# Optimization experiments

Hardware: AMD Instinct MI355X
Metric: run time of the kernel (lower is better)

The kernel has to match this reference:

```python
import jax, jax.numpy as jnp
import numpy as np

B, N, D = 2, 1024, 512
H, DH = 8, 64
HD = H * DH
FF = 2048
DEPTH = 4
SCALE = DH ** -0.5


def layer_norm(x, g, b, eps=1e-5):
    m = jnp.mean(x, axis=-1, keepdims=True)
    v = jnp.mean((x - m) ** 2, axis=-1, keepdims=True)
    return (x - m) / jnp.sqrt(v + eps) * g + b


def rel_shift(x):
    # x: (i, j, b, h) -> Transformer-XL relative shift via pad/reshape/slice
    i, j = x.shape[0], x.shape[1]
    zp = jnp.zeros((i, 1) + x.shape[2:], x.dtype)
    xp = jnp.concatenate([zp, x], axis=1).reshape((j + 1, i) + x.shape[2:])
    return xp[1:].reshape(x.shape)


def setup_inputs() -> dict:
    key = jax.random.key(0)
    ks = jax.random.split(key, 20)
    s = 0.02
    inp = {
        'x':   jax.random.normal(ks[0], (B, N, D), jnp.float32),
        'r_t': jax.random.normal(ks[1], (B, N, D), jnp.float32),
        'r_c': jax.random.normal(ks[2], (B, N, D), jnp.float32),
        'r_p': jax.random.normal(ks[3], (B, N, D), jnp.float32),
        'bias_pf': jax.random.normal(ks[4], (H, DH), jnp.float32) * s,
        'ln1_g': jnp.ones((DEPTH, D), jnp.float32),
        'ln1_b': jnp.zeros((DEPTH, D), jnp.float32),
        'w_qkv': jax.random.normal(ks[5], (DEPTH, D, 3 * HD), jnp.float32) * s,
        'w_out': jax.random.normal(ks[6], (DEPTH, HD, D), jnp.float32) * s,
        'b_out': jnp.zeros((DEPTH, D), jnp.float32),
        'w_kt': jax.random.normal(ks[7], (DEPTH, D, HD), jnp.float32) * s,
        'w_kc': jax.random.normal(ks[8], (DEPTH, D, HD), jnp.float32) * s,
        'w_kp': jax.random.normal(ks[9], (DEPTH, D, HD), jnp.float32) * s,
        'ln2_g': jnp.ones((DEPTH, D), jnp.float32),
        'ln2_b': jnp.zeros((DEPTH, D), jnp.float32),
        'w_ff1': jax.random.normal(ks[10], (DEPTH, D, FF), jnp.float32) * s,
        'b_ff1': jnp.zeros((DEPTH, FF), jnp.float32),
        'w_ff2': jax.random.normal(ks[11], (DEPTH, FF, D), jnp.float32) * s,
        'b_ff2': jnp.zeros((DEPTH, D), jnp.float32),
    }
    return inp


def _to_nbhd(t, b, n):
    # (b, n, h*d) -> (n, b, h, d)
    return t.reshape(b, n, H, DH).transpose(1, 0, 2, 3)


def reference(x, r_t, r_c, r_p, bias_pf, ln1_g, ln1_b, w_qkv, w_out, b_out,
              w_kt, w_kc, w_kp, ln2_g, ln2_b, w_ff1, b_ff1, w_ff2, b_ff2):
    b, n, _ = x.shape
    attn_last = None
    for l in range(DEPTH):
        xn = layer_norm(x, ln1_g[l], ln1_b[l])
        qkv = xn @ w_qkv[l]  # (b, n, 3*HD)
        q, k, v = jnp.split(qkv, 3, axis=-1)
        q = _to_nbhd(q, b, n) + bias_pf  # Ex_Wq + bias_pf, (n,b,h,d)
        k = _to_nbhd(k, b, n)
        v = _to_nbhd(v, b, n)
        wt = _to_nbhd(r_t @ w_kt[l], b, n)
        wc = _to_nbhd(r_c @ w_kc[l], b, n)
        wp = _to_nbhd(r_p @ w_kp[l], b, n)
        AC = jnp.einsum('ibhd,jbhd->ijbh', q, k)
        BD = (rel_shift(jnp.einsum('ibhd,jbhd->ijbh', q, wt))
              + rel_shift(jnp.einsum('ibhd,jbhd->ijbh', q, wc))
              + rel_shift(jnp.einsum('ibhd,jbhd->ijbh', q, wp))) * (1.0 / 3.0)
        dots = (AC + BD) * SCALE
        # NOTE: source uses nn.Softmax(dim=-1) on (i,j,b,h), i.e. over heads.
        attn = jax.nn.softmax(dots, axis=-1)
        out = jnp.einsum('ijbh,jbhd->ibhd', attn, v)
        out = out.transpose(1, 0, 2, 3).reshape(b, n, HD)
        x = out @ w_out[l] + b_out[l] + x
        xn2 = layer_norm(x, ln2_g[l], ln2_b[l])
        h1 = jax.nn.gelu(xn2 @ w_ff1[l] + b_ff1[l], approximate=False)
        x = h1 @ w_ff2[l] + b_ff2[l] + x
        attn_last = attn
    # attention rearranged 'q k b h -> b h q k'
    return x, attn_last.transpose(2, 3, 0, 1)
```

## Files before the change

### kernel.cpp

```cpp
#include <hip/hip_runtime.h>
#include <hip/hip_bf16.h>


using bf16 = __hip_bfloat16;
typedef __attribute__((ext_vector_type(8))) short short8;
typedef __attribute__((ext_vector_type(4))) float float4v;
typedef __attribute__((ext_vector_type(2))) unsigned int uint2v;

__device__ __forceinline__ float ldsel(const void* p, long long i, bool isbf) {
    return isbf ? __bfloat162float(((const bf16*)p)[i]) : ((const float*)p)[i];
}
__device__ __forceinline__ void stsel(void* p, long long i, bool isbf, float v) {
    if (isbf) ((bf16*)p)[i] = __float2bfloat16(v);
    else      ((float*)p)[i] = v;
}
__device__ __forceinline__ float bf2f(short u) {
    return __uint_as_float(((unsigned)(unsigned short)u) << 16);
}
__device__ __forceinline__ short f2bf(float f) {
    bf16 h = __float2bfloat16(f);
    return *reinterpret_cast<short*>(&h);
}

__global__ void detect_kernel(const unsigned int* __restrict__ g, int* __restrict__ flag) {
    if (threadIdx.x == 0) flag[0] = ((g[0] & 0xFFFFu) != 0u) ? 1 : 0;
}

__global__ __launch_bounds__(256) void cast_in(const void* __restrict__ in, float* __restrict__ out,
                                               int n8, const int* __restrict__ flagp) {
    bool bf = flagp[0] != 0;
    int i = blockIdx.x * 256 + threadIdx.x;
    if (i >= n8) return;
    long long b = (long long)i * 8;
    if (bf) {
        short8 v = *(const short8*)((const bf16*)in + b);
        float4v o0, o1;
        #pragma unroll
        for (int j = 0; j < 4; ++j) { o0[j] = bf2f(v[j]); o1[j] = bf2f(v[4 + j]); }
        *(float4v*)(out + b) = o0;
        *(float4v*)(out + b + 4) = o1;
    } else {
        float4v a0 = *(const float4v*)((const float*)in + b);
        float4v a1 = *(const float4v*)((const float*)in + b + 4);
        *(float4v*)(out + b) = a0;
        *(float4v*)(out + b + 4) = a1;
    }
}
__global__ __launch_bounds__(256) void cast_out(const float* __restrict__ in, void* __restrict__ out,
                                                int n8, const int* __restrict__ flagp) {
    bool bf = flagp[0] != 0;
    int i = blockIdx.x * 256 + threadIdx.x;
    if (i >= n8) return;
    long long b = (long long)i * 8;
    float4v a0 = *(const float4v*)(in + b);
    float4v a1 = *(const float4v*)(in + b + 4);
    if (bf) {
        short8 v;
        #pragma unroll
        for (int j = 0; j < 4; ++j) { v[j] = f2bf(a0[j]); v[4 + j] = f2bf(a1[j]); }
        *(short8*)((bf16*)out + b) = v;
    } else {
        *(float4v*)((float*)out + b) = a0;
        *(float4v*)((float*)out + b + 4) = a1;
    }
}

__global__ __launch_bounds__(256) void attn_out(const bf16* __restrict__ attn,
                                                void* __restrict__ out,
                                                const int* __restrict__ flagp) {
    bool bf = flagp[0] != 0;
    long long e = ((long long)blockIdx.x * 256 + threadIdx.x) * 8;
    short8 v = *(const short8*)(attn + e);
    if (bf) {
        *(short8*)((bf16*)out + 1048576 + e) = v;
    } else {
        float4v o0, o1;
        #pragma unroll
        for (int j = 0; j < 4; ++j) { o0[j] = bf2f(v[j]); o1[j] = bf2f(v[4 + j]); }
        float* op = (float*)out + 1048576 + e;
        *(float4v*)op = o0;
        *(float4v*)(op + 4) = o1;
    }
}

__global__ __launch_bounds__(256) void rcat_all(const void* __restrict__ r0, const void* __restrict__ r1,
                                                const void* __restrict__ r2, bf16* __restrict__ dst,
                                                const int* __restrict__ flagp) {
    bool bf = flagp[0] != 0;
    int s = blockIdx.y;
    const void* src = (s == 0) ? r0 : ((s == 1) ? r1 : r2);
    int i = blockIdx.x * 256 + threadIdx.x;
    int m = i >> 6, k8 = (i & 63) * 8;
    long long b = (long long)m * 512 + k8;
    short8 v;
    if (bf) {
        v = *(const short8*)((const bf16*)src + b);
    } else {
        float4v a0 = *(const float4v*)((const float*)src + b);
        float4v a1 = *(const float4v*)((const float*)src + b + 4);
        #pragma unroll
        for (int j = 0; j < 4; ++j) { v[j] = f2bf(a0[j]); v[4 + j] = f2bf(a1[j]); }
    }
    *(short8*)(dst + (size_t)m * 1536 + s * 512 + k8) = v;
}

__global__ __launch_bounds__(256) void prep_weights(
    const void* __restrict__ s0, const void* __restrict__ s1, const void* __restrict__ s2,
    const void* __restrict__ s3, const void* __restrict__ s4, const void* __restrict__ s5,
    const void* __restrict__ s6, bf16* __restrict__ arena,
    const int* __restrict__ flagp) {
    const bool bf = flagp[0] != 0;
    const int bid = blockIdx.x;
    const int l = bid / 960;
    const int rem = bid - l * 960;
    const int LW = 3932160;
    const int L = l * LW;

    int j, tile, tx, ldi, ldo;
    long long ioff;
    int dstoff;
    if (rem < 192)      { j = 0; tile = rem;                tx = 24; ldi = 1536; ldo = 512;
                          ioff = (long long)l * 786432;  dstoff = L; }
    else if (rem < 448) { j = 1 + ((rem - 192) >> 6); tile = (rem - 192) & 63; tx = 8; ldi = 512;
                          ioff = (long long)l * 262144;
                          if (j <= 3) { ldo = 1536; dstoff = L + 786432 + (j - 1) * 512; }
                          else        { ldo = 512;  dstoff = L + 1572864; } }
    else if (rem < 704) { j = 5; tile = rem - 448;          tx = 32; ldi = 2048; ldo = 512;
                          ioff = (long long)l * 1048576; dstoff = L + 1835008; }
    else                { j = 6; tile = rem - 704;          tx = 8;  ldi = 512;  ldo = 2048;
                          ioff = (long long)l * 1048576; dstoff = L + 2883584; }
    const void* in = (j == 0) ? s0 : (j == 1) ? s1 : (j == 2) ? s2 :
                     (j == 3) ? s3 : (j == 4) ? s4 : (j == 5) ? s5 : s6;
    bf16* out = arena + dstoff;
    const int bx = tile % tx, by = tile / tx;
    const int n0 = bx * 64, k0 = by * 64;
    const int tid = threadIdx.x;

    __shared__ bf16 t[64][72];

    if (bf) {
        const bf16* inb = (const bf16*)in + ioff;
        #pragma unroll
        for (int p = 0; p < 2; ++p) {
            int e = tid + p * 256;
            int r = e >> 3, c = (e & 7) * 8;
            *(uint4*)&t[r][c] = *(const uint4*)(inb + (size_t)(k0 + r) * ldi + n0 + c);
        }
    } else {
        const float* inf = (const float*)in + ioff;
        #pragma unroll
        for (int p = 0; p < 4; ++p) {
            int e = tid + p * 256;
            int r = e >> 4, c = (e & 15) * 4;
            float4v v = *(const float4v*)(inf + (size_t)(k0 + r) * ldi + n0 + c);
            union { bf16 h[4]; uint2v u; } w;
            #pragma unroll
            for (int q = 0; q < 4; ++q) w.h[q] = __float2bfloat16(v[q]);
            *reinterpret_cast<uint2v*>(&t[r][c]) = w.u;
        }
    }
    __syncthreads();
    #pragma unroll
    for (int p = 0; p < 2; ++p) {
        int e = tid + p * 256;
        int r = e >> 3, c = (e & 7) * 8;
        union { short8 s; uint4 u; } o;
        #pragma unroll
        for (int q = 0; q < 8; ++q)
            o.s[q] = *reinterpret_cast<const short*>(&t[c + q][r]);
        *(uint4*)(out + (size_t)(n0 + r) * ldo + k0 + c) = o.u;
    }
}

__global__ __launch_bounds__(256) void ln_kernel(const float* __restrict__ x,
                                                 const void* __restrict__ g, long long goff,
                                                 const void* __restrict__ bta, long long boff,
                                                 bf16* __restrict__ out,
                                                 const int* __restrict__ flagp) {
    bool bf = flagp[0] != 0;
    int row = blockIdx.x;
    const float* xr = x + (size_t)row * 512;
    int tid = threadIdx.x;
    float v0 = xr[tid], v1 = xr[tid + 256];
    float s = v0 + v1, q = v0 * v0 + v1 * v1;
    #pragma unroll
    for (int off = 32; off; off >>= 1) {
        s += __shfl_down(s, off);
        q += __shfl_down(q, off);
    }
    __shared__ float ls[4], lq[4];
    int wid = tid >> 6, lane = tid & 63;
    if (lane == 0) { ls[wid] = s; lq[wid] = q; }
    __syncthreads();
    if (tid == 0) {
        float ts = ls[0] + ls[1] + ls[2] + ls[3];
        float tq = lq[0] + lq[1] + lq[2] + lq[3];
        float m = ts * (1.f / 512.f);
        float var = tq * (1.f / 512.f) - m * m;
        ls[0] = m; lq[0] = rsqrtf(var + 1e-5f);
    }
    __syncthreads();
    float m = ls[0], r = lq[0];
    out[(size_t)row * 512 + tid] =
        __float2bfloat16((v0 - m) * r * ldsel(g, goff + tid, bf) + ldsel(bta, boff + tid, bf));
    out[(size_t)row * 512 + tid + 256] =
        __float2bfloat16((v1 - m) * r * ldsel(g, goff + tid + 256, bf) + ldsel(bta, boff + tid + 256, bf));
}

template<int EPI>
__global__ __launch_bounds__(256) void mgemm(
    const bf16* __restrict__ A, int lda, long long sAb, long long sAh,
    const bf16* __restrict__ B, int ldb, long long sBb, long long sBh,
    void* __restrict__ Cv, int ldc, long long sCb, long long sCh,
    int K,
    const void* __restrict__ bias, long long biasoff,
    float* __restrict__ resid,
    bf16* __restrict__ aux,
    const int* __restrict__ flagp) {
    const bool flg = flagp[0] != 0;
    const int tid = threadIdx.x;
    const int lane = tid & 63, wave = tid >> 6;
    const int m0 = blockIdx.y * 128, n0 = blockIdx.x * 64;
    const int zb = (int)(blockIdx.z >> 3), zh = (int)(blockIdx.z & 7);
    A += (size_t)zb * sAb + (size_t)zh * sAh;
    B += (size_t)zb * sBb + (size_t)zh * sBh;

    __shared__ bf16 As[128][40];
    __shared__ bf16 Bs[64][40];

    const int ar = tid >> 2, ak = (tid & 3) * 8;
    const bf16* Ap0 = A + (size_t)(m0 + ar) * lda + ak;
    const bf16* Ap1 = Ap0 + (size_t)64 * lda;
    const bf16* Bp  = B + (size_t)(n0 + ar) * ldb + ak;

    const int wm = (wave >> 1) * 64, wn = (wave & 1) * 32;
    const int fr = lane & 15, fq = lane >> 4;

    float4v acc[4][2] = {};

    uint4 a0 = *(const uint4*)Ap0;
    uint4 a1 = *(const uint4*)Ap1;
    uint4 b0 = *(const uint4*)Bp;

    for (int k0 = 0; k0 < K; k0 += 32) {
        __syncthreads();
        *(uint4*)&As[ar][ak]      = a0;
        *(uint4*)&As[ar + 64][ak] = a1;
        *(uint4*)&Bs[ar][ak]      = b0;
        if (k0 + 32 < K) {
            a0 = *(const uint4*)(Ap0 + k0 + 32);
            a1 = *(const uint4*)(Ap1 + k0 + 32);
            b0 = *(const uint4*)(Bp + k0 + 32);
        }
        __syncthreads();
        union { uint4 u; short8 s; } ua[4], ub[2];
        #pragma unroll
        for (int i = 0; i < 4; ++i) ua[i].u = *(const uint4*)&As[wm + i * 16 + fr][fq * 8];
        #pragma unroll
        for (int j = 0; j < 2; ++j) ub[j].u = *(const uint4*)&Bs[wn + j * 16 + fr][fq * 8];
        #pragma unroll
        for (int i = 0; i < 4; ++i)
            #pragma unroll
            for (int j = 0; j < 2; ++j)
                acc[i][j] = __builtin_amdgcn_mfma_f32_16x16x32_bf16(ua[i].s, ub[j].s, acc[i][j], 0, 0, 0);
    }

    const long long coff = (long long)zb * sCb + (long long)zh * sCh;
    #pragma unroll
    for (int i = 0; i < 4; ++i) {
        #pragma unroll
        for (int j = 0; j < 2; ++j) {
            #pragma unroll
            for (int r = 0; r < 4; ++r) {
                int m = m0 + wm + i * 16 + fq * 4 + r;
                int n = n0 + wn + j * 16 + fr;
                float v = acc[i][j][r];
                if (EPI == 1) {
                    bf16* C = (bf16*)Cv;
                    if (n < 512) {
                        C[(size_t)m * ldc + n] = __float2bfloat16(v + ldsel(bias, biasoff + n, flg));
                    } else if (n < 1024) {
                        C[(size_t)m * ldc + n] = __float2bfloat16(v);
                    } else {
                        int h = (n >> 6) & 7, d = n & 63, ii = m & 1023, bb = m >> 10;
                        aux[(size_t)(bb * 8 + h) * 65536 + (size_t)d * 1024 + ii] = __float2bfloat16(v);
                    }
                } else if (EPI == 2) {
                    float* C = (float*)Cv;
                    C[(size_t)m * ldc + n] = v + ldsel(bias, biasoff + n, flg) + resid[(size_t)m * ldc + n];
                } else if (EPI == 3) {
                    bf16* C = (bf16*)Cv;
                    float t = v + ldsel(bias, biasoff + n, flg);
                    C[(size_t)m * ldc + n] = __float2bfloat16(0.5f * t * (1.f + erff(t * 0.70710678118f)));
                } else if (EPI == 5) {
                    bf16* C = (bf16*)Cv + coff;
                    C[(size_t)m * ldc + n] = __float2bfloat16(v);
                }
            }
        }
    }
}

template<int EPI>
__global__ __launch_bounds__(256) void mgemm64(
    const bf16* __restrict__ A, int lda, long long sAb, long long sAh,
    const bf16* __restrict__ B, int ldb, long long sBb, long long sBh,
    void* __restrict__ Cv, int ldc, long long sCb, long long sCh,
    int K,
    const void* __restrict__ bias, long long biasoff,
    float* __restrict__ resid,
    bf16* __restrict__ aux,
    const int* __restrict__ flagp) {
    const bool flg = flagp[0] != 0;
    const int tid = threadIdx.x;
    const int lane = tid & 63, wave = tid >> 6;
    const int m0 = blockIdx.y * 64, n0 = blockIdx.x * 64;
    const int zb = (int)(blockIdx.z >> 3), zh = (int)(blockIdx.z & 7);
    A += (size_t)zb * sAb + (size_t)zh * sAh;
    B += (size_t)zb * sBb + (size_t)zh * sBh;

    __shared__ bf16 As[64][40];
    __shared__ bf16 Bs[64][40];

    const int ar = tid >> 2, ak = (tid & 3) * 8;
    const bf16* Ap = A + (size_t)(m0 + ar) * lda + ak;
    const bf16* Bp = B + (size_t)(n0 + ar) * ldb + ak;

    const int wm = (wave >> 1) * 32, wn = (wave & 1) * 32;
    const int fr = lane & 15, fq = lane >> 4;

    float4v acc[2][2] = {};

    uint4 a0 = *(const uint4*)Ap;
    uint4 b0 = *(const uint4*)Bp;

    for (int k0 = 0; k0 < K; k0 += 32) {
        __syncthreads();
        *(uint4*)&As[ar][ak] = a0;
        *(uint4*)&Bs[ar][ak] = b0;
        if (k0 + 32 < K) {
            a0 = *(const uint4*)(Ap + k0 + 32);
            b0 = *(const uint4*)(Bp + k0 + 32);
        }
        __syncthreads();
        union { uint4 u; short8 s; } ua[2], ub[2];
        #pragma unroll
        for (int i = 0; i < 2; ++i) ua[i].u = *(const uint4*)&As[wm + i * 16 + fr][fq * 8];
        #pragma unroll
        for (int j = 0; j < 2; ++j) ub[j].u = *(const uint4*)&Bs[wn + j * 16 + fr][fq * 8];
        #pragma unroll
        for (int i = 0; i < 2; ++i)
            #pragma unroll
            for (int j = 0; j < 2; ++j)
                acc[i][j] = __builtin_amdgcn_mfma_f32_16x16x32_bf16(ua[i].s, ub[j].s, acc[i][j], 0, 0, 0);
    }

    const long long coff = (long long)zb * sCb + (long long)zh * sCh;
    #pragma unroll
    for (int i = 0; i < 2; ++i) {
        #pragma unroll
        for (int j = 0; j < 2; ++j) {
            #pragma unroll
            for (int r = 0; r < 4; ++r) {
                int m = m0 + wm + i * 16 + fq * 4 + r;
                int n = n0 + wn + j * 16 + fr;
                float v = acc[i][j][r];
                if (EPI == 1) {
                    bf16* C = (bf16*)Cv;
                    if (n < 512) {
                        C[(size_t)m * ldc + n] = __float2bfloat16(v + ldsel(bias, biasoff + n, flg));
                    } else if (n < 1024) {
                        C[(size_t)m * ldc + n] = __float2bfloat16(v);
                    } else {
                        int h = (n >> 6) & 7, d = n & 63, ii = m & 1023, bb = m >> 10;
                        aux[(size_t)(bb * 8 + h) * 65536 + (size_t)d * 1024 + ii] = __float2bfloat16(v);
                    }
                } else if (EPI == 2) {
                    float* C = (float*)Cv;
                    C[(size_t)m * ldc + n] = v + ldsel(bias, biasoff + n, flg) + resid[(size_t)m * ldc + n];
                } else if (EPI == 5) {
                    bf16* C = (bf16*)Cv + coff;
                    C[(size_t)m * ldc + n] = __float2bfloat16(v);
                }
            }
        }
    }
}

__global__ __launch_bounds__(512) void bd_kernel(
    const bf16* __restrict__ qkvb, const bf16* __restrict__ wsum,
    bf16* __restrict__ Scb) {
    const int tid = threadIdx.x;
    const int lane = tid & 63, wave = tid >> 6;
    const int n0 = blockIdx.x * 64, m0 = blockIdx.y * 64, b = blockIdx.z;

    __shared__ bf16 Qs[64][72];
    __shared__ bf16 Ws[64][72];

    const int r0 = tid >> 3, c0 = (tid & 7) * 8;
    const bf16* Qp = qkvb + (size_t)(b * 1024 + m0 + r0) * 1536 + c0;
    const bf16* Wp = wsum + (size_t)(b * 1024 + n0 + r0) * 512 + c0;

    const int wm = (wave >> 2) * 32, wn = (wave & 3) * 16;
    const int fr = lane & 15, fq = lane >> 4;

    float4v acc[8][2] = {};

    uint4 qreg = *(const uint4*)Qp;
    uint4 wreg = *(const uint4*)Wp;

    for (int h = 0; h < 8; ++h) {
        __syncthreads();
        *(uint4*)&Qs[r0][c0] = qreg;
        *(uint4*)&Ws[r0][c0] = wreg;
        if (h < 7) {
            qreg = *(const uint4*)(Qp + (h + 1) * 64);
            wreg = *(const uint4*)(Wp + (h + 1) * 64);
        }
        __syncthreads();
        #pragma unroll
        for (int ks = 0; ks < 2; ++ks) {
            union { uint4 u; short8 s; } ua[2], ub;
            #pragma unroll
            for (int i = 0; i < 2; ++i) ua[i].u = *(const uint4*)&Qs[wm + i * 16 + fr][fq * 8 + ks * 32];
            ub.u = *(const uint4*)&Ws[wn + fr][fq * 8 + ks * 32];
            #pragma unroll
            for (int i = 0; i < 2; ++i)
                acc[h][i] = __builtin_amdgcn_mfma_f32_16x16x32_bf16(ua[i].s, ub.s, acc[h][i], 0, 0, 0);
        }
    }

    const size_t pb = (size_t)b * 8388608;
    #pragma unroll
    for (int i = 0; i < 2; ++i) {
        #pragma unroll
        for (int r = 0; r < 4; ++r) {
            int m = m0 + wm + i * 16 + fq * 4 + r;
            int n = n0 + wn + fr;
            int t = m * 1025 + n + 1;
            if (t >= 1024) {
                short8 v;
                #pragma unroll
                for (int h = 0; h < 8; ++h) v[h] = f2bf(acc[h][i][r] * (1.f / 3.f));
                *(short8*)(Scb + pb + (size_t)(t - 1024) * 8) = v;
            }
        }
    }
}

__global__ __launch_bounds__(512) void scores_kernel(
    const bf16* __restrict__ qkvb, const bf16* __restrict__ Scb,
    bf16* __restrict__ attn) {
    const int tid = threadIdx.x;
    const int lane = tid & 63, wave = tid >> 6;
    const int j0 = blockIdx.x * 64, i0 = blockIdx.y * 64, b = blockIdx.z;

    __shared__ bf16 Qs[64][72];
    __shared__ bf16 Ks[64][72];

    const int r0 = tid >> 3, c0 = (tid & 7) * 8;
    const bf16* Qp = qkvb + (size_t)(b * 1024 + i0 + r0) * 1536 + c0;
    const bf16* Kp = qkvb + (size_t)(b * 1024 + j0 + r0) * 1536 + 512 + c0;

    const int wm = (wave >> 2) * 32, wn = (wave & 3) * 16;
    const int fr = lane & 15, fq = lane >> 4;

    float4v acc[8][2] = {};

    uint4 qreg = *(const uint4*)Qp;
    uint4 kreg = *(const uint4*)Kp;

    for (int h = 0; h < 8; ++h) {
        __syncthreads();
        *(uint4*)&Qs[r0][c0] = qreg;
        *(uint4*)&Ks[r0][c0] = kreg;
        if (h < 7) {
            qreg = *(const uint4*)(Qp + (h + 1) * 64);
            kreg = *(const uint4*)(Kp + (h + 1) * 64);
        }
        __syncthreads();
        #pragma unroll
        for (int ks = 0; ks < 2; ++ks) {
            union { uint4 u; short8 s; } ua[2], ub;
            #pragma unroll
            for (int i = 0; i < 2; ++i) ua[i].u = *(const uint4*)&Qs[wm + i * 16 + fr][fq * 8 + ks * 32];
            ub.u = *(const uint4*)&Ks[wn + fr][fq * 8 + ks * 32];
            #pragma unroll
            for (int i = 0; i < 2; ++i)
                acc[h][i] = __builtin_amdgcn_mfma_f32_16x16x32_bf16(ua[i].s, ub.s, acc[h][i], 0, 0, 0);
        }
    }

    short8 bdv[8];
    float mxs[8], invs[8];
    const size_t pb = (size_t)b * 8388608;
    #pragma unroll
    for (int i = 0; i < 2; ++i) {
        #pragma unroll
        for (int r = 0; r < 4; ++r) {
            const int e = i * 4 + r;
            int gi = i0 + wm + i * 16 + fq * 4 + r;
            int gj = j0 + wn + fr;
            bdv[e] = *(const short8*)(Scb + pb + ((size_t)gi * 1024 + gj) * 8);
            bool diag = (gj == gi + 1);
            float dv[8];
            float mx = -3.4e38f;
            #pragma unroll
            for (int h = 0; h < 8; ++h) {
                float bd = diag ? 0.f : bf2f(bdv[e][h]);
                dv[h] = (acc[h][i][r] + bd) * 0.125f;
                mx = fmaxf(mx, dv[h]);
            }
            float s = 0.f;
            #pragma unroll
            for (int h = 0; h < 8; ++h) s += __expf(dv[h] - mx);
            mxs[e] = mx; invs[e] = 1.f / s;
        }
    }

    const size_t ab = (size_t)b * 8388608;
    const int orow = tid >> 3, ocol = (tid & 7) * 8;
    #pragma unroll
    for (int h = 0; h < 8; ++h) {
        __syncthreads();
        #pragma unroll
        for (int i = 0; i < 2; ++i) {
            #pragma unroll
            for (int r = 0; r < 4; ++r) {
                const int e = i * 4 + r;
                int gil = wm + i * 16 + fq * 4 + r;
                int gjl = wn + fr;
                int gi = i0 + gil, gj = j0 + gjl;
                float bd = (gj == gi + 1) ? 0.f : bf2f(bdv[e][h]);
                float a = __expf((acc[h][i][r] + bd) * 0.125f - mxs[e]) * invs[e];
                Qs[gil][gjl] = __float2bfloat16(a);
            }
        }
        __syncthreads();
        *(uint4*)(attn + ab + (size_t)h * 1048576 + (size_t)(i0 + orow) * 1024 + j0 + ocol)
            = *(const uint4*)&Qs[orow][ocol];
    }
}

extern "C" void kernel_launch(void* const* d_in, const int* in_sizes, int n_in,
                              void* d_out, int out_size, void* d_ws, size_t ws_size,
                              hipStream_t stream) {
    (void)in_sizes; (void)n_in; (void)out_size; (void)ws_size;
    const void* x_in    = d_in[0];
    const void* r_t     = d_in[1];
    const void* r_c     = d_in[2];
    const void* r_p     = d_in[3];
    const void* bias_pf = d_in[4];
    const void* ln1_g   = d_in[5];
    const void* ln1_b   = d_in[6];
    const void* w_qkv   = d_in[7];
    const void* w_outw  = d_in[8];
    const void* b_out   = d_in[9];
    const void* w_kt    = d_in[10];
    const void* w_kc    = d_in[11];
    const void* w_kp    = d_in[12];
    const void* ln2_g   = d_in[13];
    const void* ln2_b   = d_in[14];
    const void* w_ff1   = d_in[15];
    const void* b_ff1   = d_in[16];
    const void* w_ff2   = d_in[17];
    const void* b_ff2   = d_in[18];

    float* xbuf  = (float*)d_ws;
    bf16* base16 = (bf16*)(xbuf + 1048576);
    bf16* Scb   = base16;
    bf16* h1    = base16;
    bf16* attn  = base16 + 16777216;
    bf16* xnb   = attn + 16777216;
    bf16* qkvb  = xnb + 1048576;
    bf16* vT    = qkvb + 3145728;
    bf16* wsum4 = vT + 1048576;
    bf16* rcat  = wsum4 + 4194304;
    bf16* arena = rcat + 3145728;
    int*  flagp = (int*)(arena + 15728640);

    const int LW = 3932160;
    const int WCAT_O = 786432, OUT_O = 1572864, FF1_O = 1835008, FF2_O = 2883584;
    const int QKV_O = 0;

    dim3 blk(256), blk8(512);

    detect_kernel<<<1, 64, 0, stream>>>((const unsigned int*)ln1_g, flagp);
    cast_in<<<512, blk, 0, stream>>>(x_in, xbuf, 131072, flagp);
    rcat_all<<<dim3(512, 3), blk, 0, stream>>>(r_t, r_c, r_p, rcat, flagp);

    prep_weights<<<3840, blk, 0, stream>>>(
        w_qkv, w_kt, w_kc, w_kp, w_outw, w_ff1, w_ff2, arena, flagp);

    mgemm64<5><<<dim3(8, 32, 4), blk, 0, stream>>>(
        rcat, 1536, 0, 0, arena + WCAT_O, 1536, 0, LW,
        wsum4, 512, 0, 1048576, 1536, nullptr, 0, nullptr, nullptr, flagp);

    for (int l = 0; l < 4; ++l) {
        const bf16* qkvT  = arena + l * LW + QKV_O;
        const bf16* outT  = arena + l * LW + OUT_O;
        const bf16* ff1T  = arena + l * LW + FF1_O;
        const bf16* ff2T  = arena + l * LW + FF2_O;
        const bf16* wsum  = wsum4 + (size_t)l * 1048576;

        ln_kernel<<<2048, blk, 0, stream>>>(xbuf, ln1_g, l * 512, ln1_b, l * 512, xnb, flagp);
        mgemm64<1><<<dim3(24, 32, 1), blk, 0, stream>>>(
            xnb, 512, 0, 0, qkvT, 512, 0, 0,
            qkvb, 1536, 0, 0, 512, bias_pf, 0, nullptr, vT, flagp);
        bd_kernel<<<dim3(16, 16, 2), blk8, 0, stream>>>(qkvb, wsum, Scb);
        scores_kernel<<<dim3(16, 16, 2), blk8, 0, stream>>>(qkvb, Scb, attn);
        mgemm64<5><<<dim3(1, 16, 16), blk, 0, stream>>>(
            attn, 1024, 8388608, 1048576, vT, 1024, 524288, 65536,
            xnb, 512, 524288, 64, 1024, nullptr, 0, nullptr, nullptr, flagp);
        mgemm64<2><<<dim3(8, 32, 1), blk, 0, stream>>>(
            xnb, 512, 0, 0, outT, 512, 0, 0,
            xbuf, 512, 0, 0, 512, b_out, (long long)l * 512, xbuf, nullptr, flagp);
        ln_kernel<<<2048, blk, 0, stream>>>(xbuf, ln2_g, l * 512, ln2_b, l * 512, xnb, flagp);
        mgemm<3><<<dim3(32, 16, 1), blk, 0, stream>>>(
            xnb, 512, 0, 0, ff1T, 512, 0, 0,
            h1, 2048, 0, 0, 512, b_ff1, (long long)l * 2048, nullptr, nullptr, flagp);
        mgemm64<2><<<dim3(8, 32, 1), blk, 0, stream>>>(
            h1, 2048, 0, 0, ff2T, 2048, 0, 0,
            xbuf, 512, 0, 0, 2048, b_ff2, (long long)l * 512, xbuf, nullptr, flagp);
    }

    attn_out<<<8192, blk, 0, stream>>>(attn, d_out, flagp);
    cast_out<<<512, blk, 0, stream>>>(xbuf, d_out, 131072, flagp);
}
```

Before: 715.1 us.

## Fuse layernorm into QKV and FF1 GEMMs and merge input/output cast kernels

Removes the two per-layer layernorm kernels by computing row mean/variance and normalizing each 64-row A tile straight into shared memory inside a new GEMM kernel used for the QKV and FF1 projections. The input-cast and r-concatenation kernels are merged into one launch, and the two output copy kernels into another, cutting launch count and the xnb round trip through global memory. In exchange, every column block recomputes the layernorm for its rows, reading fp32 activations redundantly, and the FF1 GEMM drops from 128-row to 64-row tiles with a large shared-memory A buffer, which may lower occupancy.

Measured after the change: 865.1 us. +21.0%, slower.

```diff
diff --git a/kernel.cpp b/kernel.cpp
--- a/kernel.cpp
+++ b/kernel.cpp
@@ -10,10 +10,6 @@
 __device__ __forceinline__ float ldsel(const void* p, long long i, bool isbf) {
     return isbf ? __bfloat162float(((const bf16*)p)[i]) : ((const float*)p)[i];
 }
-__device__ __forceinline__ void stsel(void* p, long long i, bool isbf, float v) {
-    if (isbf) ((bf16*)p)[i] = __float2bfloat16(v);
-    else      ((float*)p)[i] = v;
-}
 __device__ __forceinline__ float bf2f(short u) {
     return __uint_as_float(((unsigned)(unsigned short)u) << 16);
 }
@@ -26,82 +22,79 @@
     if (threadIdx.x == 0) flag[0] = ((g[0] & 0xFFFFu) != 0u) ? 1 : 0;
 }
 
-__global__ __launch_bounds__(256) void cast_in(const void* __restrict__ in, float* __restrict__ out,
-                                               int n8, const int* __restrict__ flagp) {
+__global__ __launch_bounds__(256) void input_prep(
+    const void* __restrict__ x_in, const void* __restrict__ r0,
+    const void* __restrict__ r1, const void* __restrict__ r2,
+    float* __restrict__ xbuf, bf16* __restrict__ rcat,
+    const int* __restrict__ flagp) {
     bool bf = flagp[0] != 0;
+    int y = blockIdx.y;
     int i = blockIdx.x * 256 + threadIdx.x;
-    if (i >= n8) return;
-    long long b = (long long)i * 8;
-    if (bf) {
-        short8 v = *(const short8*)((const bf16*)in + b);
-        float4v o0, o1;
-        #pragma unroll
-        for (int j = 0; j < 4; ++j) { o0[j] = bf2f(v[j]); o1[j] = bf2f(v[4 + j]); }
-        *(float4v*)(out + b) = o0;
-        *(float4v*)(out + b + 4) = o1;
+    if (y == 0) {
+        long long b = (long long)i * 8;
+        if (bf) {
+            short8 v = *(const short8*)((const bf16*)x_in + b);
+            float4v o0, o1;
+            #pragma unroll
+            for (int j = 0; j < 4; ++j) { o0[j] = bf2f(v[j]); o1[j] = bf2f(v[4 + j]); }
+            *(float4v*)(xbuf + b) = o0;
+            *(float4v*)(xbuf + b + 4) = o1;
+        } else {
+            float4v a0 = *(const float4v*)((const float*)x_in + b);
+            float4v a1 = *(const float4v*)((const float*)x_in + b + 4);
+            *(float4v*)(xbuf + b) = a0;
+            *(float4v*)(xbuf + b + 4) = a1;
+        }
     } else {
-        float4v a0 = *(const float4v*)((const float*)in + b);
-        float4v a1 = *(const float4v*)((const float*)in + b + 4);
-        *(float4v*)(out + b) = a0;
-        *(float4v*)(out + b + 4) = a1;
-    }
-}
-__global__ __launch_bounds__(256) void cast_out(const float* __restrict__ in, void* __restrict__ out,
-                                                int n8, const int* __restrict__ flagp) {
+        int s = y - 1;
+        const void* src = (s == 0) ? r0 : ((s == 1) ? r1 : r2);
+        int m = i >> 6, k8 = (i & 63) * 8;
+        long long b = (long long)m * 512 + k8;
+        short8 v;
+        if (bf) {
+            v = *(const short8*)((const bf16*)src + b);
+        } else {
+            float4v a0 = *(const float4v*)((const float*)src + b);
+            float4v a1 = *(const float4v*)((const float*)src + b + 4);
+            #pragma unroll
+            for (int j = 0; j < 4; ++j) { v[j] = f2bf(a0[j]); v[4 + j] = f2bf(a1[j]); }
+        }
+        *(short8*)(rcat + (size_t)m * 1536 + s * 512 + k8) = v;
+    }
+}
+
+__global__ __launch_bounds__(256) void outputs_kernel(
+    const float* __restrict__ xbuf, const bf16* __restrict__ attn,
+    void* __restrict__ out, const int* __restrict__ flagp) {
     bool bf = flagp[0] != 0;
-    int i = blockIdx.x * 256 + threadIdx.x;
-    if (i >= n8) return;
-    long long b = (long long)i * 8;
-    float4v a0 = *(const float4v*)(in + b);
-    float4v a1 = *(const float4v*)(in + b + 4);
-    if (bf) {
-        short8 v;
-        #pragma unroll
-        for (int j = 0; j < 4; ++j) { v[j] = f2bf(a0[j]); v[4 + j] = f2bf(a1[j]); }
-        *(short8*)((bf16*)out + b) = v;
+    int bid = blockIdx.x;
+    if (bid < 512) {
+        long long b = ((long long)bid * 256 + threadIdx.x) * 8;
+        float4v a0 = *(const float4v*)(xbuf + b);
+        float4v a1 = *(const float4v*)(xbuf + b + 4);
+        if (bf) {
+            short8 v;
+            #pragma unroll
+            for (int j = 0; j < 4; ++j) { v[j] = f2bf(a0[j]); v[4 + j] = f2bf(a1[j]); }
+            *(short8*)((bf16*)out + b) = v;
+        } else {
+            *(float4v*)((float*)out + b) = a0;
+            *(float4v*)((float*)out + b + 4) = a1;
+        }
     } else {
-        *(float4v*)((float*)out + b) = a0;
-        *(float4v*)((float*)out + b + 4) = a1;
-    }
-}
-
-__global__ __launch_bounds__(256) void attn_out(const bf16* __restrict__ attn,
-                                                void* __restrict__ out,
-                                                const int* __restrict__ flagp) {
-    bool bf = flagp[0] != 0;
-    long long e = ((long long)blockIdx.x * 256 + threadIdx.x) * 8;
-    short8 v = *(const short8*)(attn + e);
-    if (bf) {
-        *(short8*)((bf16*)out + 1048576 + e) = v;
-    } else {
-        float4v o0, o1;
-        #pragma unroll
-        for (int j = 0; j < 4; ++j) { o0[j] = bf2f(v[j]); o1[j] = bf2f(v[4 + j]); }
-        float* op = (float*)out + 1048576 + e;
-        *(float4v*)op = o0;
-        *(float4v*)(op + 4) = o1;
-    }
-}
-
-__global__ __launch_bounds__(256) void rcat_all(const void* __restrict__ r0, const void* __restrict__ r1,
-                                                const void* __restrict__ r2, bf16* __restrict__ dst,
-                                                const int* __restrict__ flagp) {
-    bool bf = flagp[0] != 0;
-    int s = blockIdx.y;
-    const void* src = (s == 0) ? r0 : ((s == 1) ? r1 : r2);
-    int i = blockIdx.x * 256 + threadIdx.x;
-    int m = i >> 6, k8 = (i & 63) * 8;
-    long long b = (long long)m * 512 + k8;
-    short8 v;
-    if (bf) {
-        v = *(const short8*)((const bf16*)src + b);
-    } else {
-        float4v a0 = *(const float4v*)((const float*)src + b);
-        float4v a1 = *(const float4v*)((const float*)src + b + 4);
-        #pragma unroll
-        for (int j = 0; j < 4; ++j) { v[j] = f2bf(a0[j]); v[4 + j] = f2bf(a1[j]); }
-    }
-    *(short8*)(dst + (size_t)m * 1536 + s * 512 + k8) = v;
+        long long e = ((long long)(bid - 512) * 256 + threadIdx.x) * 8;
+        short8 v = *(const short8*)(attn + e);
+        if (bf) {
+            *(short8*)((bf16*)out + 1048576 + e) = v;
+        } else {
+            float4v o0, o1;
+            #pragma unroll
+            for (int j = 0; j < 4; ++j) { o0[j] = bf2f(v[j]); o1[j] = bf2f(v[4 + j]); }
+            float* op = (float*)out + 1048576 + e;
+            *(float4v*)op = o0;
+            *(float4v*)(op + 4) = o1;
+        }
+    }
 }
 
 __global__ __launch_bounds__(256) void prep_weights(
@@ -169,135 +162,6 @@
         for (int q = 0; q < 8; ++q)
             o.s[q] = *reinterpret_cast<const short*>(&t[c + q][r]);
         *(uint4*)(out + (size_t)(n0 + r) * ldo + k0 + c) = o.u;
-    }
-}
-
-__global__ __launch_bounds__(256) void ln_kernel(const float* __restrict__ x,
-                                                 const void* __restrict__ g, long long goff,
-                                                 const void* __restrict__ bta, long long boff,
-                                                 bf16* __restrict__ out,
-                                                 const int* __restrict__ flagp) {
-    bool bf = flagp[0] != 0;
-    int row = blockIdx.x;
-    const float* xr = x + (size_t)row * 512;
-    int tid = threadIdx.x;
-    float v0 = xr[tid], v1 = xr[tid + 256];
-    float s = v0 + v1, q = v0 * v0 + v1 * v1;
-    #pragma unroll
-    for (int off = 32; off; off >>= 1) {
-        s += __shfl_down(s, off);
-        q += __shfl_down(q, off);
-    }
-    __shared__ float ls[4], lq[4];
-    int wid = tid >> 6, lane = tid & 63;
-    if (lane == 0) { ls[wid] = s; lq[wid] = q; }
-    __syncthreads();
-    if (tid == 0) {
-        float ts = ls[0] + ls[1] + ls[2] + ls[3];
-        float tq = lq[0] + lq[1] + lq[2] + lq[3];
-        float m = ts * (1.f / 512.f);
-        float var = tq * (1.f / 512.f) - m * m;
-        ls[0] = m; lq[0] = rsqrtf(var + 1e-5f);
-    }
-    __syncthreads();
-    float m = ls[0], r = lq[0];
-    out[(size_t)row * 512 + tid] =
-        __float2bfloat16((v0 - m) * r * ldsel(g, goff + tid, bf) + ldsel(bta, boff + tid, bf));
-    out[(size_t)row * 512 + tid + 256] =
-        __float2bfloat16((v1 - m) * r * ldsel(g, goff + tid + 256, bf) + ldsel(bta, boff + tid + 256, bf));
-}
-
-template<int EPI>
-__global__ __launch_bounds__(256) void mgemm(
-    const bf16* __restrict__ A, int lda, long long sAb, long long sAh,
-    const bf16* __restrict__ B, int ldb, long long sBb, long long sBh,
-    void* __restrict__ Cv, int ldc, long long sCb, long long sCh,
-    int K,
-    const void* __restrict__ bias, long long biasoff,
-    float* __restrict__ resid,
-    bf16* __restrict__ aux,
-    const int* __restrict__ flagp) {
-    const bool flg = flagp[0] != 0;
-    const int tid = threadIdx.x;
-    const int lane = tid & 63, wave = tid >> 6;
-    const int m0 = blockIdx.y * 128, n0 = blockIdx.x * 64;
-    const int zb = (int)(blockIdx.z >> 3), zh = (int)(blockIdx.z & 7);
-    A += (size_t)zb * sAb + (size_t)zh * sAh;
-    B += (size_t)zb * sBb + (size_t)zh * sBh;
-
-    __shared__ bf16 As[128][40];
-    __shared__ bf16 Bs[64][40];
-
-    const int ar = tid >> 2, ak = (tid & 3) * 8;
-    const bf16* Ap0 = A + (size_t)(m0 + ar) * lda + ak;
-    const bf16* Ap1 = Ap0 + (size_t)64 * lda;
-    const bf16* Bp  = B + (size_t)(n0 + ar) * ldb + ak;
-
-    const int wm = (wave >> 1) * 64, wn = (wave & 1) * 32;
-    const int fr = lane & 15, fq = lane >> 4;
-
-    float4v acc[4][2] = {};
-
-    uint4 a0 = *(const uint4*)Ap0;
-    uint4 a1 = *(const uint4*)Ap1;
-    uint4 b0 = *(const uint4*)Bp;
-
-    for (int k0 = 0; k0 < K; k0 += 32) {
-        __syncthreads();
-        *(uint4*)&As[ar][ak]      = a0;
-        *(uint4*)&As[ar + 64][ak] = a1;
-        *(uint4*)&Bs[ar][ak]      = b0;
-        if (k0 + 32 < K) {
-            a0 = *(const uint4*)(Ap0 + k0 + 32);
-            a1 = *(const uint4*)(Ap1 + k0 + 32);
-            b0 = *(const uint4*)(Bp + k0 + 32);
-        }
-        __syncthreads();
-        union { uint4 u; short8 s; } ua[4], ub[2];
-        #pragma unroll
-        for (int i = 0; i < 4; ++i) ua[i].u = *(const uint4*)&As[wm + i * 16 + fr][fq * 8];
-        #pragma unroll
-        for (int j = 0; j < 2; ++j) ub[j].u = *(const uint4*)&Bs[wn + j * 16 + fr][fq * 8];
-        #pragma unroll
-        for (int i = 0; i < 4; ++i)
-            #pragma unroll
-            for (int j = 0; j < 2; ++j)
-                acc[i][j] = __builtin_amdgcn_mfma_f32_16x16x32_bf16(ua[i].s, ub[j].s, acc[i][j], 0, 0, 0);
-    }
-
-    const long long coff = (long long)zb * sCb + (long long)zh * sCh;
-    #pragma unroll
-    for (int i = 0; i < 4; ++i) {
-        #pragma unroll
-        for (int j = 0; j < 2; ++j) {
-            #pragma unroll
-            for (int r = 0; r < 4; ++r) {
-                int m = m0 + wm + i * 16 + fq * 4 + r;
-                int n = n0 + wn + j * 16 + fr;
-                float v = acc[i][j][r];
-                if (EPI == 1) {
-                    bf16* C = (bf16*)Cv;
-                    if (n < 512) {
-                        C[(size_t)m * ldc + n] = __float2bfloat16(v + ldsel(bias, biasoff + n, flg));
-                    } else if (n < 1024) {
-                        C[(size_t)m * ldc + n] = __float2bfloat16(v);
-                    } else {
-                        int h = (n >> 6) & 7, d = n & 63, ii = m & 1023, bb = m >> 10;
-                        aux[(size_t)(bb * 8 + h) * 65536 + (size_t)d * 1024 + ii] = __float2bfloat16(v);
-                    }
-                } else if (EPI == 2) {
-                    float* C = (float*)Cv;
-                    C[(size_t)m * ldc + n] = v + ldsel(bias, biasoff + n, flg) + resid[(size_t)m * ldc + n];
-                } else if (EPI == 3) {
-                    bf16* C = (bf16*)Cv;
-                    float t = v + ldsel(bias, biasoff + n, flg);
-                    C[(size_t)m * ldc + n] = __float2bfloat16(0.5f * t * (1.f + erff(t * 0.70710678118f)));
-                } else if (EPI == 5) {
-                    bf16* C = (bf16*)Cv + coff;
-                    C[(size_t)m * ldc + n] = __float2bfloat16(v);
-                }
-            }
-        }
     }
 }
 
@@ -381,6 +245,113 @@
                 } else if (EPI == 5) {
                     bf16* C = (bf16*)Cv + coff;
                     C[(size_t)m * ldc + n] = __float2bfloat16(v);
+                }
+            }
+        }
+    }
+}
+
+template<int EPI>
+__global__ __launch_bounds__(256) void mgemm_ln(
+    const float* __restrict__ A,
+    const void* __restrict__ g, long long goff,
+    const void* __restrict__ bta, long long boff,
+    const bf16* __restrict__ B, int ldb,
+    void* __restrict__ Cv, int ldc,
+    const void* __restrict__ bias, long long biasoff,
+    bf16* __restrict__ aux,
+    const int* __restrict__ flagp) {
+    const bool flg = flagp[0] != 0;
+    const int tid = threadIdx.x;
+    const int lane = tid & 63, wave = tid >> 6;
+    const int m0 = blockIdx.y * 64, n0 = blockIdx.x * 64;
+
+    __shared__ bf16 As[64][524];
+    __shared__ bf16 Bs[64][40];
+    __shared__ float gs[512], bs[512];
+
+    const int ar = tid >> 2, ak = (tid & 3) * 8;
+    const bf16* Bp = B + (size_t)(n0 + ar) * ldb + ak;
+    uint4 b0 = *(const uint4*)Bp;
+
+    gs[tid]       = ldsel(g,   goff + tid, flg);
+    gs[tid + 256] = ldsel(g,   goff + tid + 256, flg);
+    bs[tid]       = ldsel(bta, boff + tid, flg);
+    bs[tid + 256] = ldsel(bta, boff + tid + 256, flg);
+
+    const int r = tid >> 2, qc = tid & 3;
+    const float* xr = A + (size_t)(m0 + r) * 512 + qc * 128;
+    float s = 0.f, q = 0.f;
+    #pragma unroll
+    for (int c = 0; c < 128; c += 4) {
+        float4v v = *(const float4v*)(xr + c);
+        #pragma unroll
+        for (int u = 0; u < 4; ++u) { s += v[u]; q += v[u] * v[u]; }
+    }
+    s += __shfl_xor(s, 1); q += __shfl_xor(q, 1);
+    s += __shfl_xor(s, 2); q += __shfl_xor(q, 2);
+    const float mean = s * (1.f / 512.f);
+    const float rstd = rsqrtf(q * (1.f / 512.f) - mean * mean + 1e-5f);
+
+    __syncthreads();
+    #pragma unroll
+    for (int c = 0; c < 128; c += 8) {
+        float4v v0 = *(const float4v*)(xr + c);
+        float4v v1 = *(const float4v*)(xr + c + 4);
+        union { bf16 h[8]; uint4 u; } w;
+        #pragma unroll
+        for (int u = 0; u < 4; ++u) {
+            int cc = qc * 128 + c + u;
+            w.h[u]     = __float2bfloat16((v0[u] - mean) * rstd * gs[cc] + bs[cc]);
+            w.h[4 + u] = __float2bfloat16((v1[u] - mean) * rstd * gs[cc + 4] + bs[cc + 4]);
+        }
+        *(uint4*)&As[r][qc * 128 + c] = w.u;
+    }
+
+    const int wm = (wave >> 1) * 32, wn = (wave & 1) * 32;
+    const int fr = lane & 15, fq = lane >> 4;
+    float4v acc[2][2] = {};
+
+    for (int k0 = 0; k0 < 512; k0 += 32) {
+        __syncthreads();
+        *(uint4*)&Bs[ar][ak] = b0;
+        if (k0 + 32 < 512) b0 = *(const uint4*)(Bp + k0 + 32);
+        __syncthreads();
+        union { uint4 u; short8 s; } ua[2], ub[2];
+        #pragma unroll
+        for (int i = 0; i < 2; ++i) ua[i].u = *(const uint4*)&As[wm + i * 16 + fr][fq * 8 + k0];
+        #pragma unroll
+        for (int j = 0; j < 2; ++j) ub[j].u = *(const uint4*)&Bs[wn + j * 16 + fr][fq * 8];
+        #pragma unroll
+        for (int i = 0; i < 2; ++i)
+            #pragma unroll
+            for (int j = 0; j < 2; ++j)
+                acc[i][j] = __builtin_amdgcn_mfma_f32_16x16x32_bf16(ua[i].s, ub[j].s, acc[i][j], 0, 0, 0);
+    }
+
+    #pragma unroll
+    for (int i = 0; i < 2; ++i) {
+        #pragma unroll
+        for (int j = 0; j < 2; ++j) {
+            #pragma unroll
+            for (int rr = 0; rr < 4; ++rr) {
+                int m = m0 + wm + i * 16 + fq * 4 + rr;
+                int n = n0 + wn + j * 16 + fr;
+                float v = acc[i][j][rr];
+                if (EPI == 1) {
+                    bf16* C = (bf16*)Cv;
+                    if (n < 512) {
+                        C[(size_t)m * ldc + n] = __float2bfloat16(v + ldsel(bias, biasoff + n, flg));
+                    } else if (n < 1024) {
+                        C[(size_t)m * ldc + n] = __float2bfloat16(v);
+                    } else {
+                        int h = (n >> 6) & 7, d = n & 63, ii = m & 1023, bb = m >> 10;
+                        aux[(size_t)(bb * 8 + h) * 65536 + (size_t)d * 1024 + ii] = __float2bfloat16(v);
+                    }
+                } else if (EPI == 3) {
+                    bf16* C = (bf16*)Cv;
+                    float t = v + ldsel(bias, biasoff + n, flg);
+                    C[(size_t)m * ldc + n] = __float2bfloat16(0.5f * t * (1.f + erff(t * 0.70710678118f)));
                 }
             }
         }
@@ -586,8 +557,7 @@
     dim3 blk(256), blk8(512);
 
     detect_kernel<<<1, 64, 0, stream>>>((const unsigned int*)ln1_g, flagp);
-    cast_in<<<512, blk, 0, stream>>>(x_in, xbuf, 131072, flagp);
-    rcat_all<<<dim3(512, 3), blk, 0, stream>>>(r_t, r_c, r_p, rcat, flagp);
+    input_prep<<<dim3(512, 4), blk, 0, stream>>>(x_in, r_t, r_c, r_p, xbuf, rcat, flagp);
 
     prep_weights<<<3840, blk, 0, stream>>>(
         w_qkv, w_kt, w_kc, w_kp, w_outw, w_ff1, w_ff2, arena, flagp);
@@ -603,10 +573,9 @@
         const bf16* ff2T  = arena + l * LW + FF2_O;
         const bf16* wsum  = wsum4 + (size_t)l * 1048576;
 
-        ln_kernel<<<2048, blk, 0, stream>>>(xbuf, ln1_g, l * 512, ln1_b, l * 512, xnb, flagp);
-        mgemm64<1><<<dim3(24, 32, 1), blk, 0, stream>>>(
-            xnb, 512, 0, 0, qkvT, 512, 0, 0,
-            qkvb, 1536, 0, 0, 512, bias_pf, 0, nullptr, vT, flagp);
+        mgemm_ln<1><<<dim3(24, 32), blk, 0, stream>>>(
+            xbuf, ln1_g, l * 512, ln1_b, l * 512,
+            qkvT, 512, qkvb, 1536, bias_pf, 0, vT, flagp);
         bd_kernel<<<dim3(16, 16, 2), blk8, 0, stream>>>(qkvb, wsum, Scb);
         scores_kernel<<<dim3(16, 16, 2), blk8, 0, stream>>>(qkvb, Scb, attn);
         mgemm64<5><<<dim3(1, 16, 16), blk, 0, stream>>>(
@@ -615,15 +584,13 @@
         mgemm64<2><<<dim3(8, 32, 1), blk, 0, stream>>>(
             xnb, 512, 0, 0, outT, 512, 0, 0,
             xbuf, 512, 0, 0, 512, b_out, (long long)l * 512, xbuf, nullptr, flagp);
-        ln_kernel<<<2048, blk, 0, stream>>>(xbuf, ln2_g, l * 512, ln2_b, l * 512, xnb, flagp);
-        mgemm<3><<<dim3(32, 16, 1), blk, 0, stream>>>(
-            xnb, 512, 0, 0, ff1T, 512, 0, 0,
-            h1, 2048, 0, 0, 512, b_ff1, (long long)l * 2048, nullptr, nullptr, flagp);
+        mgemm_ln<3><<<dim3(32, 32), blk, 0, stream>>>(
+            xbuf, ln2_g, l * 512, ln2_b, l * 512,
+            ff1T, 512, h1, 2048, b_ff1, (long long)l * 2048, nullptr, flagp);
         mgemm64<2><<<dim3(8, 32, 1), blk, 0, stream>>>(
             h1, 2048, 0, 0, ff2T, 2048, 0, 0,
             xbuf, 512, 0, 0, 2048, b_ff2, (long long)l * 512, xbuf, nullptr, flagp);
     }
 
-    attn_out<<<8192, blk, 0, stream>>>(attn, d_out, flagp);
-    cast_out<<<512, blk, 0, stream>>>(xbuf, d_out, 131072, flagp);
-}
+    outputs_kernel<<<8704, blk, 0, stream>>>(xbuf, attn, d_out, flagp);
+}
```
